# Optimization experiments

Measured on AMD Instinct MI355X. Metric: run time of the kernel, lower is better.

## Reference

```python
import jax, jax.numpy as jnp
import numpy as np

NUM_HEADS = 16
HEAD_DIM = 64
KERNEL = 13  # odd
DIM = NUM_HEADS * HEAD_DIM
SCALE = HEAD_DIM ** -0.5


def setup_inputs() -> dict:
    key = jax.random.key(0)
    ks = jax.random.split(key, 6)
    B, L = 4, 4096
    return {
        "x": jax.random.normal(ks[0], (B, L, DIM), jnp.float32),
        "w_qkv": jax.random.normal(ks[1], (DIM, 3 * DIM), jnp.float32) * 0.02,
        "b_qkv": jax.random.normal(ks[2], (3 * DIM,), jnp.float32) * 0.02,
        "rpb": jax.random.normal(ks[3], (NUM_HEADS, 2 * KERNEL - 1), jnp.float32) * 0.02,
        "w_proj": jax.random.normal(ks[4], (DIM, DIM), jnp.float32) * 0.02,
        "b_proj": jax.random.normal(ks[5], (DIM,), jnp.float32) * 0.02,
    }


def _na1d(q, k, v, rpb, kernel_size):
    # q,k,v: [B,H,L,D]; rpb: [H, 2K-1]. dilation == 1.
    L = q.shape[2]
    K = kernel_size
    r = K // 2
    i = jnp.arange(L)
    # neighborhood start, clamped so each query sees exactly K keys (NATTEN semantics)
    ni = jnp.clip(i - r, 0, L - K)                    # [L]
    nbr = ni[:, None] + jnp.arange(K)                 # [L,K] key indices
    k_nb = k[:, :, nbr]                               # [B,H,L,K,D]
    attn = jnp.einsum("bhld,bhlkd->bhlk", q, k_nb)   # windowed QK
    # relative-position-bias start index: bias idx = (key_pos - i) + (K-1)
    pi = ni - i + (K - 1)                             # [L]
    bias = rpb[:, pi[:, None] + jnp.arange(K)]        # [H,L,K]
    attn = jax.nn.softmax(attn + bias[None], axis=-1)
    v_nb = v[:, :, nbr]                               # [B,H,L,K,D]
    return jnp.einsum("bhlk,bhlkd->bhld", attn, v_nb)


def reference(x, w_qkv, b_qkv, rpb, w_proj, b_proj):
    B, L, C = x.shape
    qkv = x @ w_qkv + b_qkv                           # [B,L,3C]
    qkv = qkv.reshape(B, L, 3, NUM_HEADS, HEAD_DIM).transpose(2, 0, 3, 1, 4)
    q, k, v = qkv[0] * SCALE, qkv[1], qkv[2]          # [B,H,L,D]
    out = _na1d(q, k, v, rpb, KERNEL)                 # [B,H,L,D]
    out = out.transpose(0, 2, 1, 3).reshape(B, L, C)
    return out @ w_proj + b_proj
```

## Files before the change

### kernel.cpp

```cpp
#include <hip/hip_runtime.h>

typedef __bf16 bf16x8_t __attribute__((ext_vector_type(8)));
typedef float  f32x4_t  __attribute__((ext_vector_type(4)));
typedef float  floatx4  __attribute__((ext_vector_type(4)));
typedef unsigned short ushortx4 __attribute__((ext_vector_type(4)));

__device__ __forceinline__ float bf2f(unsigned short u) {
    union { unsigned int i; float f; } c; c.i = ((unsigned int)u) << 16; return c.f;
}
__device__ __forceinline__ unsigned short f2bf(float f) {
    union { float f; unsigned int i; } c; c.f = f;
    unsigned int u = c.i;
    u += 0x7fffu + ((u >> 16) & 1u);
    return (unsigned short)(u >> 16);
}
__device__ __forceinline__ void cvt8(uint4 u, floatx4& lo, floatx4& hi) {
    union { unsigned int i; float f; } c;
    c.i = u.x << 16;          lo.x = c.f;
    c.i = u.x & 0xffff0000u;  lo.y = c.f;
    c.i = u.y << 16;          lo.z = c.f;
    c.i = u.y & 0xffff0000u;  lo.w = c.f;
    c.i = u.z << 16;          hi.x = c.f;
    c.i = u.z & 0xffff0000u;  hi.y = c.f;
    c.i = u.w << 16;          hi.z = c.f;
    c.i = u.w & 0xffff0000u;  hi.w = c.f;
}

__device__ __forceinline__ void load_lds16(const unsigned short* g, unsigned short* l) {
    __builtin_amdgcn_global_load_lds(
        (const __attribute__((address_space(1))) unsigned int*)g,
        (__attribute__((address_space(3))) unsigned int*)l, 16, 0, 0);
}

__global__ __launch_bounds__(256) void convert_f32_bf16(
    const float* __restrict__ x, unsigned short* __restrict__ xb)
{
    size_t i = ((size_t)blockIdx.x * 256 + threadIdx.x) * 8;
    floatx4 a = *reinterpret_cast<const floatx4*>(x + i);
    floatx4 b = *reinterpret_cast<const floatx4*>(x + i + 4);
    uint4 o;
    o.x = (unsigned int)f2bf(a.x) | ((unsigned int)f2bf(a.y) << 16);
    o.y = (unsigned int)f2bf(a.z) | ((unsigned int)f2bf(a.w) << 16);
    o.z = (unsigned int)f2bf(b.x) | ((unsigned int)f2bf(b.y) << 16);
    o.w = (unsigned int)f2bf(b.z) | ((unsigned int)f2bf(b.w) << 16);
    *reinterpret_cast<uint4*>(xb + i) = o;
}

__global__ __launch_bounds__(256) void transpose_f32_to_bf16(
    const float* __restrict__ W, unsigned short* __restrict__ Wt,
    int Kdim, int Ndim)
{
    __shared__ float tile[32][33];
    const int n0 = blockIdx.x * 32, k0 = blockIdx.y * 32;
    const int tx = threadIdx.x & 31, ty = threadIdx.x >> 5;
#pragma unroll
    for (int r = 0; r < 4; ++r) {
        int k = ty + r * 8;
        tile[k][tx] = W[(size_t)(k0 + k) * Ndim + n0 + tx];
    }
    __syncthreads();
#pragma unroll
    for (int r = 0; r < 4; ++r) {
        int n = ty + r * 8;
        Wt[(size_t)(n0 + n) * Kdim + k0 + tx] = f2bf(tile[tx][n]);
    }
}

#define TBM 256
#define TBN 256
#define TBK 32

template<bool C_F32>
__global__ __launch_bounds__(512, 2) void gemm_pipe_kernel(
    const unsigned short* __restrict__ A, const unsigned short* __restrict__ Wt,
    const float* __restrict__ bias, void* __restrict__ Cp,
    int N, int K, int lda, int ldc)
{
    __shared__ __align__(16) unsigned short SMEM[8][8192];

    const int tid  = threadIdx.x;
    const int lane = tid & 63;
    const int wid  = tid >> 6;
    const int wm   = wid >> 2;
    const int wn   = wid & 3;
    const int quad = lane >> 4;
    const int lr   = lane & 15;

    const int gx  = gridDim.x;
    const int cpx = (gx * gridDim.y) >> 3;
    const int bid = blockIdx.y * gx + blockIdx.x;
    const int nid = (bid & 7) * cpx + (bid >> 3);
    const int m0 = (nid / gx) * TBM;
    const int n0 = (nid % gx) * TBN;

    const int s_row = tid >> 2;
    const int c_sw  = ((tid & 3) ^ ((tid >> 3) & 3)) * 8;
    const int xq    = (quad ^ ((lr >> 1) & 3)) * 8;
    const int NT    = K >> 5;

    const unsigned short* Ag  = A  + (size_t)(m0 + s_row) * lda + c_sw;
    const unsigned short* Ag2 = Ag + (size_t)128 * lda;
    const unsigned short* Bg  = Wt + (size_t)(n0 + s_row) * K + c_sw;
    const unsigned short* Bg2 = Bg + (size_t)128 * K;

    f32x4_t acc[8][4];
#pragma unroll
    for (int i = 0; i < 8; ++i)
#pragma unroll
        for (int j = 0; j < 4; ++j)
            acc[i][j] = (f32x4_t){0.f, 0.f, 0.f, 0.f};

#pragma unroll
    for (int tt = 0; tt < 3; ++tt) {
        load_lds16(Ag  + tt * TBK, &SMEM[tt][wid * 512]);
        load_lds16(Ag2 + tt * TBK, &SMEM[tt][4096 + wid * 512]);
        load_lds16(Bg  + tt * TBK, &SMEM[4 + tt][wid * 512]);
        load_lds16(Bg2 + tt * TBK, &SMEM[4 + tt][4096 + wid * 512]);
    }
    asm volatile("s_waitcnt vmcnt(8)" ::: "memory");
    __builtin_amdgcn_s_barrier();

    for (int tt = 0; tt < NT; ++tt) {
        const int b = tt & 3;
        const unsigned short* pa = &SMEM[b][0];
        const unsigned short* pb = &SMEM[4 + b][0];
        const bool st = (tt + 3) < NT;
        const int  sb = (tt + 3) & 3;
        const int  ko = (tt + 3) * TBK;

        if (st) {
            load_lds16(Ag  + ko, &SMEM[sb][wid * 512]);
            load_lds16(Ag2 + ko, &SMEM[sb][4096 + wid * 512]);
            load_lds16(Bg  + ko, &SMEM[4 + sb][wid * 512]);
            load_lds16(Bg2 + ko, &SMEM[4 + sb][4096 + wid * 512]);
        }

        bf16x8_t bv[4], av[8];
#pragma unroll
        for (int j = 0; j < 4; ++j)
            bv[j] = *reinterpret_cast<const bf16x8_t*>(pb + (wn * 64 + j * 16 + lr) * TBK + xq);
#pragma unroll
        for (int i = 0; i < 8; ++i)
            av[i] = *reinterpret_cast<const bf16x8_t*>(pa + (wm * 128 + i * 16 + lr) * TBK + xq);

        __builtin_amdgcn_s_setprio(1);
#pragma unroll
        for (int i = 0; i < 8; ++i)
#pragma unroll
            for (int j = 0; j < 4; ++j)
                acc[i][j] = __builtin_amdgcn_mfma_f32_16x16x32_bf16(av[i], bv[j], acc[i][j], 0, 0, 0);
        __builtin_amdgcn_s_setprio(0);

        if (tt < NT - 3)       asm volatile("s_waitcnt vmcnt(8)" ::: "memory");
        else if (tt == NT - 3) asm volatile("s_waitcnt vmcnt(4)" ::: "memory");
        else                   asm volatile("s_waitcnt vmcnt(0)" ::: "memory");
        __builtin_amdgcn_s_barrier();
    }

    if (C_F32) {
#pragma unroll
        for (int j = 0; j < 4; ++j) {
            int col = n0 + wn * 64 + j * 16 + lr;
            float bj = bias[col];
#pragma unroll
            for (int i = 0; i < 8; ++i) {
                int rbase = m0 + wm * 128 + i * 16 + quad * 4;
#pragma unroll
                for (int r = 0; r < 4; ++r) {
                    float v = acc[i][j][r] + bj;
                    ((float*)Cp)[(size_t)(rbase + r) * ldc + col] = v;
                }
            }
        }
    } else {
        unsigned short* ep = &SMEM[wid][0];
#pragma unroll
        for (int j = 0; j < 4; ++j) {
            float bj = bias[n0 + wn * 64 + j * 16 + lr];
#pragma unroll
            for (int i = 0; i < 8; ++i) {
#pragma unroll
                for (int r = 0; r < 4; ++r) {
                    int row = i * 16 + quad * 4 + r;
                    int col = j * 16 + lr;
                    int ch  = (col >> 3) ^ (row & 7);
                    ep[row * 64 + ch * 8 + (col & 7)] = f2bf(acc[i][j][r] + bj);
                }
            }
        }
        unsigned short* Cb = (unsigned short*)Cp;
        const int cch = lane & 7;
#pragma unroll
        for (int s = 0; s < 16; ++s) {
            int row = s * 8 + (lane >> 3);
            int ch  = cch ^ (row & 7);
            uint4 v = *reinterpret_cast<const uint4*>(&ep[row * 64 + ch * 8]);
            *reinterpret_cast<uint4*>(
                Cb + (size_t)(m0 + wm * 128 + row) * ldc + n0 + wn * 64 + cch * 8) = v;
        }
    }
}

#define BM 128
#define BN 128
#define BK 32
#define LDT 40

template<bool A_F32, bool C_F32, bool BT>
__global__ __launch_bounds__(256) void gemm_bias_kernel(
    const void* __restrict__ Ap, const void* __restrict__ Wp,
    const float* __restrict__ bias, void* __restrict__ Cp,
    int N, int K, int lda, int ldc)
{
    __shared__ __align__(16) unsigned short As[BM * LDT];
    __shared__ __align__(16) unsigned short Bs[BN * LDT];

    const int tid  = threadIdx.x;
    const int lane = tid & 63;
    const int wid  = tid >> 6;
    const int wm   = wid >> 1;
    const int wn   = wid & 1;
    const int quad = lane >> 4;
    const int lr   = lane & 15;

    const int m0 = blockIdx.y * BM;
    const int n0 = blockIdx.x * BN;

    f32x4_t acc[4][4];
#pragma unroll
    for (int i = 0; i < 4; ++i)
#pragma unroll
        for (int j = 0; j < 4; ++j)
            acc[i][j] = (f32x4_t){0.f, 0.f, 0.f, 0.f};

    for (int k0 = 0; k0 < K; k0 += BK) {
        if (A_F32) {
            const float* A = (const float*)Ap;
#pragma unroll
            for (int it = 0; it < 4; ++it) {
                int q   = tid + it * 256;
                int row = q >> 3;
                int col = (q & 7) * 4;
                floatx4 f = *reinterpret_cast<const floatx4*>(A + (size_t)(m0 + row) * lda + k0 + col);
                ushortx4 s;
                s.x = f2bf(f.x); s.y = f2bf(f.y); s.z = f2bf(f.z); s.w = f2bf(f.w);
                *reinterpret_cast<ushortx4*>(&As[row * LDT + col]) = s;
            }
        } else {
            const unsigned short* A = (const unsigned short*)Ap;
            int a_row = tid >> 2;
            int a_col = (tid & 3) * 8;
#pragma unroll
            for (int r = 0; r < 2; ++r) {
                int row = a_row + r * 64;
                uint4 u = *reinterpret_cast<const uint4*>(A + (size_t)(m0 + row) * lda + k0 + a_col);
                *reinterpret_cast<uint4*>(&As[row * LDT + a_col]) = u;
            }
        }
        if (BT) {
            const unsigned short* Wt = (const unsigned short*)Wp;
            int b_row = tid >> 2;
            int b_col = (tid & 3) * 8;
#pragma unroll
            for (int r = 0; r < 2; ++r) {
                int n = b_row + r * 64;
                uint4 u = *reinterpret_cast<const uint4*>(Wt + (size_t)(n0 + n) * K + k0 + b_col);
                *reinterpret_cast<uint4*>(&Bs[n * LDT + b_col]) = u;
            }
        } else {
            const float* W = (const float*)Wp;
#pragma unroll
            for (int it = 0; it < 4; ++it) {
                int q  = tid + it * 256;
                int kk = q >> 5;
                int nn = (q & 31) * 4;
                floatx4 f = *reinterpret_cast<const floatx4*>(W + (size_t)(k0 + kk) * N + n0 + nn);
                Bs[(nn + 0) * LDT + kk] = f2bf(f.x);
                Bs[(nn + 1) * LDT + kk] = f2bf(f.y);
                Bs[(nn + 2) * LDT + kk] = f2bf(f.z);
                Bs[(nn + 3) * LDT + kk] = f2bf(f.w);
            }
        }
        __syncthreads();

        bf16x8_t av[4], bv[4];
#pragma unroll
        for (int i = 0; i < 4; ++i)
            av[i] = *reinterpret_cast<const bf16x8_t*>(&As[(wm * 64 + i * 16 + lr) * LDT + quad * 8]);
#pragma unroll
        for (int j = 0; j < 4; ++j)
            bv[j] = *reinterpret_cast<const bf16x8_t*>(&Bs[(wn * 64 + j * 16 + lr) * LDT + quad * 8]);

#pragma unroll
        for (int i = 0; i < 4; ++i)
#pragma unroll
            for (int j = 0; j < 4; ++j)
                acc[i][j] = __builtin_amdgcn_mfma_f32_16x16x32_bf16(av[i], bv[j], acc[i][j], 0, 0, 0);

        __syncthreads();
    }

#pragma unroll
    for (int j = 0; j < 4; ++j) {
        int col = n0 + wn * 64 + j * 16 + lr;
        float bj = bias[col];
#pragma unroll
        for (int i = 0; i < 4; ++i) {
            int rbase = m0 + wm * 64 + i * 16 + quad * 4;
#pragma unroll
            for (int r = 0; r < 4; ++r) {
                float v = acc[i][j][r] + bj;
                size_t idx = (size_t)(rbase + r) * ldc + col;
                if (C_F32) ((float*)Cp)[idx] = v;
                else       ((unsigned short*)Cp)[idx] = f2bf(v);
            }
        }
    }
}

#define NA_L 4096
#define NA_K 13
#define NA_H 16
#define NA_D 64
#define NA_SCALE 0.125f
#define TL  64
#define WIN 76

__global__ __launch_bounds__(256) void na1d_tiled_kernel(
    unsigned short* qkv, const float* __restrict__ rpb)
{
    __shared__ __align__(16) unsigned short ks_b[WIN * 64];
    __shared__ __align__(16) unsigned short vs_b[WIN * 64];
    __shared__ __align__(16) unsigned short qs_b[TL * 64];
    __shared__ float wgt[TL][NA_K];

    const int bid = blockIdx.x;
    const int h  = bid & 15;
    const int lt = (bid >> 4) & 63;
    const int b  = bid >> 10;
    const int l0 = lt * TL;
    const int rs = l0 - 6;

    const int t = threadIdx.x;
    const size_t rowbase = (size_t)b * NA_L;

    {
        const int qr = t >> 2;
        const int qi = (t & 3) * 2;
        const unsigned short* qsrc = qkv + (rowbase + l0 + qr) * 3072 + h * 64 + qi * 8;
        uint4 q0 = *reinterpret_cast<const uint4*>(qsrc);
        uint4 q1 = *reinterpret_cast<const uint4*>(qsrc + 8);

        const int r0 = t >> 3;
        const int ci = t & 7;
        int g0 = rs + r0;      g0 = g0 < 0 ? 0 : (g0 > NA_L - 1 ? NA_L - 1 : g0);
        int g1 = rs + r0 + 32; g1 = g1 < 0 ? 0 : (g1 > NA_L - 1 ? NA_L - 1 : g1);
        const unsigned short* p0 = qkv + (rowbase + g0) * 3072 + 1024 + h * 64 + ci * 8;
        const unsigned short* p1 = qkv + (rowbase + g1) * 3072 + 1024 + h * 64 + ci * 8;
        uint4 k0 = *reinterpret_cast<const uint4*>(p0);
        uint4 v0 = *reinterpret_cast<const uint4*>(p0 + 1024);
        uint4 k1 = *reinterpret_cast<const uint4*>(p1);
        uint4 v1 = *reinterpret_cast<const uint4*>(p1 + 1024);
        uint4 k2, v2;
        if (t < 96) {
            int g2 = rs + r0 + 64; g2 = g2 < 0 ? 0 : (g2 > NA_L - 1 ? NA_L - 1 : g2);
            const unsigned short* p2 = qkv + (rowbase + g2) * 3072 + 1024 + h * 64 + ci * 8;
            k2 = *reinterpret_cast<const uint4*>(p2);
            v2 = *reinterpret_cast<const uint4*>(p2 + 1024);
        }

        const int qk = qr & 7;
        *reinterpret_cast<uint4*>(qs_b + qr * 64 + (( qi      ^ qk) * 8)) = q0;
        *reinterpret_cast<uint4*>(qs_b + qr * 64 + (((qi + 1) ^ qk) * 8)) = q1;
        const int rk = r0 & 7;
        *reinterpret_cast<uint4*>(ks_b +  r0       * 64 + ((ci ^ rk) * 8)) = k0;
        *reinterpret_cast<uint4*>(vs_b +  r0       * 64 + ((ci ^ rk) * 8)) = v0;
        *reinterpret_cast<uint4*>(ks_b + (r0 + 32) * 64 + ((ci ^ rk) * 8)) = k1;
        *reinterpret_cast<uint4*>(vs_b + (r0 + 32) * 64 + ((ci ^ rk) * 8)) = v1;
        if (t < 96) {
            *reinterpret_cast<uint4*>(ks_b + (r0 + 64) * 64 + ((ci ^ rk) * 8)) = k2;
            *reinterpret_cast<uint4*>(vs_b + (r0 + 64) * 64 + ((ci ^ rk) * 8)) = v2;
        }
    }
    __syncthreads();

    {
        const int l  = t & 63;
        const int jb = (t >> 6) * 4;
        int ig = l0 + l;
        int ni = ig - 6;
        if (ni < 0) ni = 0;
        if (ni > NA_L - NA_K) ni = NA_L - NA_K;
        int rid = ni - rs;
        int pi  = ni - ig + 12;

        int r0r = rid + jb + 0; if (r0r > WIN - 1) r0r = WIN - 1;
        int r1r = rid + jb + 1; if (r1r > WIN - 1) r1r = WIN - 1;
        int r2r = rid + jb + 2; if (r2r > WIN - 1) r2r = WIN - 1;
        int r3r = rid + jb + 3; if (r3r > WIN - 1) r3r = WIN - 1;

        const unsigned short* qrow = qs_b + l * 64;
        const unsigned short* k0p  = ks_b + r0r * 64;
        const unsigned short* k1p  = ks_b + r1r * 64;
        const unsigned short* k2p  = ks_b + r2r * 64;
        const unsigned short* k3p  = ks_b + r3r * 64;
        const int qk = l & 7;
        const int x0 = r0r & 7, x1 = r1r & 7, x2 = r2r & 7, x3 = r3r & 7;

        floatx4 a0 = {0,0,0,0}, a1 = {0,0,0,0}, a2 = {0,0,0,0}, a3 = {0,0,0,0};
#pragma unroll
        for (int c = 0; c < 8; ++c) {
            floatx4 ql, qh, kl, kh;
            cvt8(*reinterpret_cast<const uint4*>(qrow + ((c ^ qk) * 8)), ql, qh);
            cvt8(*reinterpret_cast<const uint4*>(k0p + ((c ^ x0) * 8)), kl, kh);
            a0 += ql * kl; a0 += qh * kh;
            cvt8(*reinterpret_cast<const uint4*>(k1p + ((c ^ x1) * 8)), kl, kh);
            a1 += ql * kl; a1 += qh * kh;
            cvt8(*reinterpret_cast<const uint4*>(k2p + ((c ^ x2) * 8)), kl, kh);
            a2 += ql * kl; a2 += qh * kh;
            cvt8(*reinterpret_cast<const uint4*>(k3p + ((c ^ x3) * 8)), kl, kh);
            a3 += ql * kl; a3 += qh * kh;
        }
        float s0 = (a0.x + a0.y + a0.z + a0.w) * NA_SCALE;
        float s1 = (a1.x + a1.y + a1.z + a1.w) * NA_SCALE;
        float s2 = (a2.x + a2.y + a2.z + a2.w) * NA_SCALE;
        float s3 = (a3.x + a3.y + a3.z + a3.w) * NA_SCALE;
        const float* rp = rpb + h * 25 + pi;
        if (jb + 0 < NA_K) wgt[l][jb + 0] = s0 + rp[jb + 0];
        if (jb + 1 < NA_K) wgt[l][jb + 1] = s1 + rp[jb + 1];
        if (jb + 2 < NA_K) wgt[l][jb + 2] = s2 + rp[jb + 2];
        if (jb + 3 < NA_K) wgt[l][jb + 3] = s3 + rp[jb + 3];
    }
    __syncthreads();

    if (t < TL) {
        float m = -1e30f;
#pragma unroll
        for (int j = 0; j < NA_K; ++j) m = fmaxf(m, wgt[t][j]);
        float sum = 0.f;
#pragma unroll
        for (int j = 0; j < NA_K; ++j) {
            float e = expf(wgt[t][j] - m);
            wgt[t][j] = e;
            sum += e;
        }
        float inv = 1.f / sum;
#pragma unroll
        for (int j = 0; j < NA_K; ++j) wgt[t][j] *= inv;
    }
    __syncthreads();

    {
        const int l  = t & 63;
        const int wv = t >> 6;
        int ig = l0 + l;
        int ni = ig - 6;
        if (ni < 0) ni = 0;
        if (ni > NA_L - NA_K) ni = NA_L - NA_K;
        int rid = ni - rs;
        floatx4 o0 = {0,0,0,0}, o1 = {0,0,0,0}, o2 = {0,0,0,0}, o3 = {0,0,0,0};
#pragma unroll
        for (int j = 0; j < NA_K; ++j) {
            float w = wgt[l][j];
            int r = rid + j;
            int key = r & 7;
            const unsigned short* vrow = vs_b + r * 64;
            floatx4 xl, xh;
            cvt8(*reinterpret_cast<const uint4*>(vrow + (((2 * wv)     ^ key) * 8)), xl, xh);
            o0 += w * xl; o1 += w * xh;
            cvt8(*reinterpret_cast<const uint4*>(vrow + (((2 * wv + 1) ^ key) * 8)), xl, xh);
            o2 += w * xl; o3 += w * xh;
        }
        unsigned short* dst = qkv + (rowbase + ig) * 3072 + h * 64 + wv * 16;
        uint4 p0, p1;
        p0.x = (unsigned int)f2bf(o0.x) | ((unsigned int)f2bf(o0.y) << 16);
        p0.y = (unsigned int)f2bf(o0.z) | ((unsigned int)f2bf(o0.w) << 16);
        p0.z = (unsigned int)f2bf(o1.x) | ((unsigned int)f2bf(o1.y) << 16);
        p0.w = (unsigned int)f2bf(o1.z) | ((unsigned int)f2bf(o1.w) << 16);
        p1.x = (unsigned int)f2bf(o2.x) | ((unsigned int)f2bf(o2.y) << 16);
        p1.y = (unsigned int)f2bf(o2.z) | ((unsigned int)f2bf(o2.w) << 16);
        p1.z = (unsigned int)f2bf(o3.x) | ((unsigned int)f2bf(o3.y) << 16);
        p1.w = (unsigned int)f2bf(o3.z) | ((unsigned int)f2bf(o3.w) << 16);
        *reinterpret_cast<uint4*>(dst)     = p0;
        *reinterpret_cast<uint4*>(dst + 8) = p1;
    }
}

extern "C" void kernel_launch(void* const* d_in, const int* in_sizes, int n_in,
                              void* d_out, int out_size, void* d_ws, size_t ws_size,
                              hipStream_t stream)
{
    const float* x      = (const float*)d_in[0];
    const float* w_qkv  = (const float*)d_in[1];
    const float* b_qkv  = (const float*)d_in[2];
    const float* rpb    = (const float*)d_in[3];
    const float* w_proj = (const float*)d_in[4];
    const float* b_proj = (const float*)d_in[5];
    float* out = (float*)d_out;

    const int M  = 4 * 4096;
    const int K  = 1024;
    const int N1 = 3072;
    const int N2 = 1024;

    unsigned short* qkv = (unsigned short*)d_ws;
    unsigned short* Wt1 = qkv + (size_t)M * N1;
    unsigned short* Wt2 = Wt1 + (size_t)N1 * K;
    unsigned short* xb  = Wt2 + (size_t)N2 * K;
    size_t need_mid  = ((size_t)M * N1 + (size_t)N1 * K + (size_t)N2 * K) * 2;
    size_t need_fast = need_mid + (size_t)M * K * 2;

    const int na_grid = 4 * (NA_L / TL) * NA_H;

    if (ws_size >= need_fast) {
        convert_f32_bf16<<<dim3(M * K / (256 * 8)), 256, 0, stream>>>(x, xb);
        transpose_f32_to_bf16<<<dim3(N1 / 32, K / 32), 256, 0, stream>>>(w_qkv, Wt1, K, N1);
        transpose_f32_to_bf16<<<dim3(N2 / 32, K / 32), 256, 0, stream>>>(w_proj, Wt2, K, N2);
        gemm_pipe_kernel<false><<<dim3(N1 / TBN, M / TBM), 512, 0, stream>>>(
            xb, Wt1, b_qkv, qkv, N1, K, K, N1);
        na1d_tiled_kernel<<<dim3(na_grid), 256, 0, stream>>>(qkv, rpb);
        gemm_pipe_kernel<true><<<dim3(N2 / TBN, M / TBM), 512, 0, stream>>>(
            qkv, Wt2, b_proj, out, N2, K, N1, N2);
    } else if (ws_size >= need_mid) {
        transpose_f32_to_bf16<<<dim3(N1 / 32, K / 32), 256, 0, stream>>>(w_qkv, Wt1, K, N1);
        transpose_f32_to_bf16<<<dim3(N2 / 32, K / 32), 256, 0, stream>>>(w_proj, Wt2, K, N2);
        gemm_bias_kernel<true, false, true><<<dim3(N1 / BN, M / BM), 256, 0, stream>>>(
            x, Wt1, b_qkv, qkv, N1, K, K, N1);
        na1d_tiled_kernel<<<dim3(na_grid), 256, 0, stream>>>(qkv, rpb);
        gemm_bias_kernel<false, true, true><<<dim3(N2 / BN, M / BM), 256, 0, stream>>>(
            qkv, Wt2, b_proj, out, N2, K, N1, N2);
    } else {
        gemm_bias_kernel<true, false, false><<<dim3(N1 / BN, M / BM), 256, 0, stream>>>(
            x, w_qkv, b_qkv, qkv, N1, K, K, N1);
        na1d_tiled_kernel<<<dim3(na_grid), 256, 0, stream>>>(qkv, rpb);
        gemm_bias_kernel<false, true, false><<<dim3(N2 / BN, M / BM), 256, 0, stream>>>(
            qkv, w_proj, b_proj, out, N2, K, N1, N2);
    }
}
```

Before: 347.4 us.

## Switch GEMM to TBK=64 double-buffered pipeline and remap NA block ids across XCDs

```diff
diff --git a/kernel.cpp b/kernel.cpp
--- a/kernel.cpp
+++ b/kernel.cpp
@@ -68,7 +68,7 @@
 
 #define TBM 256
 #define TBN 256
-#define TBK 32
+#define TBK 64
 
 template<bool C_F32>
 __global__ __launch_bounds__(512, 2) void gemm_pipe_kernel(
@@ -76,7 +76,7 @@
     const float* __restrict__ bias, void* __restrict__ Cp,
     int N, int K, int lda, int ldc)
 {
-    __shared__ __align__(16) unsigned short SMEM[8][8192];
+    __shared__ __align__(16) unsigned short SMEM[65536];
 
     const int tid  = threadIdx.x;
     const int lane = tid & 63;
@@ -93,15 +93,14 @@
     const int m0 = (nid / gx) * TBM;
     const int n0 = (nid % gx) * TBN;
 
-    const int s_row = tid >> 2;
-    const int c_sw  = ((tid & 3) ^ ((tid >> 3) & 3)) * 8;
-    const int xq    = (quad ^ ((lr >> 1) & 3)) * 8;
-    const int NT    = K >> 5;
-
-    const unsigned short* Ag  = A  + (size_t)(m0 + s_row) * lda + c_sw;
-    const unsigned short* Ag2 = Ag + (size_t)128 * lda;
-    const unsigned short* Bg  = Wt + (size_t)(n0 + s_row) * K + c_sw;
-    const unsigned short* Bg2 = Bg + (size_t)128 * K;
+    const int s_row8 = tid >> 3;
+    const int c_sw   = ((tid & 7) ^ (s_row8 & 7)) * 8;
+    const int NT     = K >> 6;
+
+    const unsigned short* Ag = A  + (size_t)(m0 + s_row8) * lda + c_sw;
+    const unsigned short* Bg = Wt + (size_t)(n0 + s_row8) * K   + c_sw;
+
+    const int sdst = wid * 512;
 
     f32x4_t acc[8][4];
 #pragma unroll
@@ -111,38 +110,41 @@
             acc[i][j] = (f32x4_t){0.f, 0.f, 0.f, 0.f};
 
 #pragma unroll
-    for (int tt = 0; tt < 3; ++tt) {
-        load_lds16(Ag  + tt * TBK, &SMEM[tt][wid * 512]);
-        load_lds16(Ag2 + tt * TBK, &SMEM[tt][4096 + wid * 512]);
-        load_lds16(Bg  + tt * TBK, &SMEM[4 + tt][wid * 512]);
-        load_lds16(Bg2 + tt * TBK, &SMEM[4 + tt][4096 + wid * 512]);
-    }
-    asm volatile("s_waitcnt vmcnt(8)" ::: "memory");
+    for (int r = 0; r < 4; ++r) {
+        load_lds16(Ag + (size_t)(r * 64) * lda, SMEM + r * 4096 + sdst);
+        load_lds16(Bg + (size_t)(r * 64) * K,   SMEM + 32768 + r * 4096 + sdst);
+    }
+    asm volatile("s_waitcnt vmcnt(0)" ::: "memory");
     __builtin_amdgcn_s_barrier();
 
-    for (int tt = 0; tt < NT; ++tt) {
-        const int b = tt & 3;
-        const unsigned short* pa = &SMEM[b][0];
-        const unsigned short* pb = &SMEM[4 + b][0];
-        const bool st = (tt + 3) < NT;
-        const int  sb = (tt + 3) & 3;
-        const int  ko = (tt + 3) * TBK;
-
-        if (st) {
-            load_lds16(Ag  + ko, &SMEM[sb][wid * 512]);
-            load_lds16(Ag2 + ko, &SMEM[sb][4096 + wid * 512]);
-            load_lds16(Bg  + ko, &SMEM[4 + sb][wid * 512]);
-            load_lds16(Bg2 + ko, &SMEM[4 + sb][4096 + wid * 512]);
-        }
-
-        bf16x8_t bv[4], av[8];
+    const int xk = lr & 7;
+
+    for (int tau = 0; tau < NT; ++tau) {
+        const int doff = (tau & 1) * 16384;
+        const unsigned short* pa = SMEM + doff;
+        const unsigned short* pb = SMEM + 32768 + doff;
+
+        if (tau + 1 < NT) {
+            const int noff = ((tau + 1) & 1) * 16384;
+            unsigned short* na = SMEM + noff;
+            unsigned short* nb = SMEM + 32768 + noff;
+            const size_t ko = (size_t)(tau + 1) * TBK;
+#pragma unroll
+            for (int r = 0; r < 4; ++r) {
+                load_lds16(Ag + (size_t)(r * 64) * lda + ko, na + r * 4096 + sdst);
+                load_lds16(Bg + (size_t)(r * 64) * K   + ko, nb + r * 4096 + sdst);
+            }
+        }
+
+        bf16x8_t av[8], bv[4];
 #pragma unroll
         for (int j = 0; j < 4; ++j)
-            bv[j] = *reinterpret_cast<const bf16x8_t*>(pb + (wn * 64 + j * 16 + lr) * TBK + xq);
+            bv[j] = *reinterpret_cast<const bf16x8_t*>(
+                pb + (wn * 64 + j * 16 + lr) * 64 + ((quad ^ xk) * 8));
 #pragma unroll
         for (int i = 0; i < 8; ++i)
-            av[i] = *reinterpret_cast<const bf16x8_t*>(pa + (wm * 128 + i * 16 + lr) * TBK + xq);
-
+            av[i] = *reinterpret_cast<const bf16x8_t*>(
+                pa + (wm * 128 + i * 16 + lr) * 64 + ((quad ^ xk) * 8));
         __builtin_amdgcn_s_setprio(1);
 #pragma unroll
         for (int i = 0; i < 8; ++i)
@@ -151,9 +153,23 @@
                 acc[i][j] = __builtin_amdgcn_mfma_f32_16x16x32_bf16(av[i], bv[j], acc[i][j], 0, 0, 0);
         __builtin_amdgcn_s_setprio(0);
 
-        if (tt < NT - 3)       asm volatile("s_waitcnt vmcnt(8)" ::: "memory");
-        else if (tt == NT - 3) asm volatile("s_waitcnt vmcnt(4)" ::: "memory");
-        else                   asm volatile("s_waitcnt vmcnt(0)" ::: "memory");
+#pragma unroll
+        for (int j = 0; j < 4; ++j)
+            bv[j] = *reinterpret_cast<const bf16x8_t*>(
+                pb + (wn * 64 + j * 16 + lr) * 64 + (((4 + quad) ^ xk) * 8));
+#pragma unroll
+        for (int i = 0; i < 8; ++i)
+            av[i] = *reinterpret_cast<const bf16x8_t*>(
+                pa + (wm * 128 + i * 16 + lr) * 64 + (((4 + quad) ^ xk) * 8));
+        __builtin_amdgcn_s_setprio(1);
+#pragma unroll
+        for (int i = 0; i < 8; ++i)
+#pragma unroll
+            for (int j = 0; j < 4; ++j)
+                acc[i][j] = __builtin_amdgcn_mfma_f32_16x16x32_bf16(av[i], bv[j], acc[i][j], 0, 0, 0);
+        __builtin_amdgcn_s_setprio(0);
+
+        asm volatile("s_waitcnt vmcnt(0)" ::: "memory");
         __builtin_amdgcn_s_barrier();
     }
 
@@ -173,7 +189,7 @@
             }
         }
     } else {
-        unsigned short* ep = &SMEM[wid][0];
+        unsigned short* ep = SMEM + wid * 8192;
 #pragma unroll
         for (int j = 0; j < 4; ++j) {
             float bj = bias[n0 + wn * 64 + j * 16 + lr];
@@ -334,7 +350,10 @@
     __shared__ __align__(16) unsigned short qs_b[TL * 64];
     __shared__ float wgt[TL][NA_K];
 
-    const int bid = blockIdx.x;
+    const int cpx = gridDim.x >> 3;
+    const int hb  = blockIdx.x;
+    const int bid = (hb & 7) * cpx + (hb >> 3);
+
     const int h  = bid & 15;
     const int lt = (bid >> 4) & 63;
     const int b  = bid >> 10;
```

After: 335.3 us. 1.04x faster.
